# Kernel optimization log

Hardware: AMD Instinct MI355X
Metric: run time of the kernel (lower is better)

## Reference

```python
import jax, jax.numpy as jnp
import numpy as np

B, NELEC, D, NION = 2048, 32, 512, 8
NSPIN = 2
N = NELEC // NSPIN  # electrons per spin = orbital-matrix size = 16


def setup_inputs() -> dict:
    key = jax.random.key(0)
    ks = jax.random.split(key, 6)
    eq_inputs = jax.random.normal(ks[0], (B, NELEC, D), jnp.float32)
    r_ei = jax.random.normal(ks[1], (B, NELEC, NION, 3), jnp.float32)
    # learned params (stacked over the 2 spins; equal split so shapes match)
    W_lin = jax.random.normal(ks[2], (NSPIN, 2 * D, N), jnp.float32) * (0.5 / np.sqrt(D))
    b_lin = jax.random.normal(ks[3], (NSPIN, N), jnp.float32) * 0.1
    A_env = jax.random.normal(ks[4], (NSPIN, 3, 3, NION, N), jnp.float32) * 0.3
    w_ion = jax.random.normal(ks[5], (NSPIN, NION, N), jnp.float32)
    return dict(eq_inputs=eq_inputs, r_ei=r_ei, W_lin=W_lin, b_lin=b_lin,
                A_env=A_env, w_ion=w_ion)


def reference(eq_inputs, r_ei, W_lin, b_lin, A_env, w_ion):
    """Per-particle determinant antiequivariance layer.

    For each spin s and particle p, a doubly-equivariant orbital matrix
    M_p[j, k] = (y_p . W1[:,k] + y_j . W2[:,k] + b[k]) * env[j, k]
    is built (pair-concat dense split into two einsums to avoid the (B,n,n,2d)
    intermediate), with anisotropic exponential envelopes
    env[j, k] = sum_I w_ion[I,k] * exp(-||A[:,:,I,k] @ r_ei[j,I,:]||).
    Output per spin: y_p * det(M_p), stacked over spins -> (B, 2, n, d).
    """
    b, nelec, d = eq_inputs.shape
    n = nelec // NSPIN
    x = eq_inputs.reshape(b, NSPIN, n, d)            # spin_split=2 equal split
    r = r_ei.reshape(b, NSPIN, n, r_ei.shape[-2], 3)
    W1, W2 = W_lin[:, :d], W_lin[:, d:]
    # linear (doubly equivariant) part: (B, S, n_p, n_j, n_k)
    lin_p = jnp.einsum('bspf,sfk->bspk', x, W1)
    lin_j = jnp.einsum('bsjf,sfk->bsjk', x, W2) + b_lin[None, :, None, :]
    lin = lin_p[:, :, :, None, :] + lin_j[:, :, None, :, :]
    # anisotropic exponential envelopes: exp(-||A (r - R)||), combined over ions
    ar = jnp.einsum('bsjip,spqik->bsjiqk', r, A_env)        # (B,S,n,I,3,k)
    env = jnp.exp(-jnp.sqrt(jnp.sum(ar * ar, axis=-2)))     # (B,S,n,I,k)
    env = jnp.einsum('bsjik,sik->bsjk', env, w_ion)         # (B,S,n_j,n_k)
    M = lin * env[:, :, None, :, :]                         # (B,S,n_p,n_j,n_k)
    dets = jnp.linalg.det(M)                                # (B,S,n_p)
    # y_p * det(M_p), per spin (stacked over the spin axis)
    return x * dets[..., None]                              # (B,S,n,d)
```

## Files before the change

### kernel.cpp

```cpp
#include <hip/hip_runtime.h>
#include <hip/hip_bf16.h>
#include <cstdint>
#include <cstddef>

#define NSPIN 2
#define NPART 16
#define DDIM  512
#define NION  8
#define NB    4

#define RS_OFF     0
#define GRAM_OFF   1536
#define LINP_OFF   (GRAM_OFF + 1152)
#define LINJ_OFF   (LINP_OFF + 1280)
#define ENV_OFF    (LINJ_OFF + 1280)
#define DETS_OFF   (ENV_OFF + 1280)
#define LDS_FLOATS (DETS_OFF + 64)
#define LDS_BYTES  (LDS_FLOATS * 4)

#define WS_GRAM_F  16384

typedef short bf16x8 __attribute__((ext_vector_type(8)));
typedef float f32x4  __attribute__((ext_vector_type(4)));

__device__ __forceinline__ short bfc(float x) {
    unsigned u = __float_as_uint(x);
    u += 0x7FFFu + ((u >> 16) & 1u);
    return (short)(u >> 16);
}

union AFU { bf16x8 v; __hip_bfloat162 h[4]; };

__device__ __forceinline__ bf16x8 cvt8(const float4& a, const float4& b) {
    AFU u;
    u.h[0] = __float22bfloat162_rn(make_float2(a.x, a.y));
    u.h[1] = __float22bfloat162_rn(make_float2(a.z, a.w));
    u.h[2] = __float22bfloat162_rn(make_float2(b.x, b.y));
    u.h[3] = __float22bfloat162_rn(make_float2(b.z, b.w));
    return u.v;
}

#define DPPMAXU(k, ctrl) { unsigned o_ = (unsigned)__builtin_amdgcn_update_dpp(0, (int)(k), (ctrl), 0xF, 0xF, true); (k) = (k) > o_ ? (k) : o_; }

__global__ void __launch_bounds__(256)
prep_kernel(const float* __restrict__ WL, const float* __restrict__ AE,
            const float* __restrict__ WI, float* __restrict__ WSF)
{
    const int t = threadIdx.x;
    if (blockIdx.x < 16) {
        int slot = blockIdx.x * 256 + t;
        int spin = slot >> 11;
        int rem  = slot & 2047;
        int half = rem >> 10;
        int ks   = (rem >> 6) & 15;
        int lane = rem & 63;
        int cc2  = lane & 15, hh = lane >> 4;
        const float* src = WL + (size_t)spin * (2 * DDIM * NPART)
                         + ((size_t)(half * 512 + ks * 32 + hh * 8)) * NPART + cc2;
        ushort u[8];
        #pragma unroll
        for (int e = 0; e < 8; ++e) u[e] = (ushort)bfc(src[e * NPART]);
        uint4 pk;
        pk.x = (unsigned)u[0] | ((unsigned)u[1] << 16);
        pk.y = (unsigned)u[2] | ((unsigned)u[3] << 16);
        pk.z = (unsigned)u[4] | ((unsigned)u[5] << 16);
        pk.w = (unsigned)u[6] | ((unsigned)u[7] << 16);
        ((uint4*)WSF)[slot] = pk;
    } else {
        int s  = t >> 7;
        int ke = (t >> 3) & 15;
        int i  = t & 7;
        const float* Ag = AE + (size_t)s * (9 * NION * NPART);
        float a00 = Ag[((0 * 3 + 0) * NION + i) * NPART + ke];
        float a01 = Ag[((0 * 3 + 1) * NION + i) * NPART + ke];
        float a02 = Ag[((0 * 3 + 2) * NION + i) * NPART + ke];
        float a10 = Ag[((1 * 3 + 0) * NION + i) * NPART + ke];
        float a11 = Ag[((1 * 3 + 1) * NION + i) * NPART + ke];
        float a12 = Ag[((1 * 3 + 2) * NION + i) * NPART + ke];
        float a20 = Ag[((2 * 3 + 0) * NION + i) * NPART + ke];
        float a21 = Ag[((2 * 3 + 1) * NION + i) * NPART + ke];
        float a22 = Ag[((2 * 3 + 2) * NION + i) * NPART + ke];
        float* g = WSF + WS_GRAM_F + t * 8;
        g[0] = a00 * a00 + a01 * a01 + a02 * a02;
        g[1] = a10 * a10 + a11 * a11 + a12 * a12;
        g[2] = a20 * a20 + a21 * a21 + a22 * a22;
        g[3] = a00 * a10 + a01 * a11 + a02 * a12;
        g[4] = a00 * a20 + a01 * a21 + a02 * a22;
        g[5] = a10 * a20 + a11 * a21 + a12 * a22;
        g[6] = WI[(size_t)s * (NION * NPART) + i * NPART + ke];
        g[7] = 0.f;
    }
}

__global__ void __launch_bounds__(256, 4)
ppdet_kernel(const float* __restrict__ EQ, const float* __restrict__ RE,
             const float* __restrict__ WSF, const float* __restrict__ BL,
             float* __restrict__ OUT)
{
    extern __shared__ float ls[];
    const int t  = threadIdx.x;
    const int s  = blockIdx.x >> 9;
    const int b0 = (blockIdx.x & 511) * NB;

    const int l  = t & 63;
    const int w  = t >> 6;
    const int c  = l & 15;
    const int h4 = l >> 4;
    const int jr = t & 15;
    const int ke = t >> 4;

    #pragma unroll
    for (int it = 0; it < 6; ++it) {
        int idx = it * 256 + t;
        int ibuf = idx / 384, rem = idx % 384;
        int e = rem >> 4, j = rem & 15;
        ls[RS_OFF + idx] = RE[((size_t)(b0 + ibuf) * 32 + s * 16 + j) * 24 + e];
    }
    #pragma unroll
    for (int it = 0; it < 4; ++it) {
        int idx = it * 256 + t;
        int kk = idx >> 6, rem = idx & 63;
        ls[GRAM_OFF + kk * 72 + rem] = WSF[WS_GRAM_F + s * 1024 + idx];
    }

    {
        const float* xg  = EQ + ((size_t)((b0 + w) * 32 + s * 16 + c)) * DDIM + h4 * 8;
        const uint4* wb1 = (const uint4*)WSF + (size_t)s * 2048;
        const uint4* wb2 = wb1 + 1024;
        f32x4 accp = {0.f, 0.f, 0.f, 0.f}, accj = {0.f, 0.f, 0.f, 0.f};
        float4 xA[8], xB[8];
        #pragma unroll
        for (int u = 0; u < 4; ++u) {
            xA[2 * u]     = *(const float4*)(xg + u * 32);
            xA[2 * u + 1] = *(const float4*)(xg + u * 32 + 4);
        }
        #pragma unroll
        for (int kb = 0; kb < 4; ++kb) {
            float4* cur = (kb & 1) ? xB : xA;
            float4* nxt = (kb & 1) ? xA : xB;
            if (kb < 3) {
                #pragma unroll
                for (int u = 0; u < 4; ++u) {
                    nxt[2 * u]     = *(const float4*)(xg + (kb + 1) * 128 + u * 32);
                    nxt[2 * u + 1] = *(const float4*)(xg + (kb + 1) * 128 + u * 32 + 4);
                }
            }
            uint4 w1v[4], w2v[4];
            #pragma unroll
            for (int u = 0; u < 4; ++u) {
                w1v[u] = wb1[(kb * 4 + u) * 64 + l];
                w2v[u] = wb2[(kb * 4 + u) * 64 + l];
            }
            #pragma unroll
            for (int u = 0; u < 4; ++u) {
                bf16x8 af = cvt8(cur[2 * u], cur[2 * u + 1]);
                accp = __builtin_amdgcn_mfma_f32_16x16x32_bf16(af, *(bf16x8*)&w1v[u], accp, 0, 0, 0);
                accj = __builtin_amdgcn_mfma_f32_16x16x32_bf16(af, *(bf16x8*)&w2v[u], accj, 0, 0, 0);
            }
        }
        const float blv = BL[s * NPART + c];
        #pragma unroll
        for (int q = 0; q < 4; ++q) {
            ls[LINP_OFF + (w * 16 + h4 * 4 + q) * 20 + c] = accp[q];
            ls[LINJ_OFF + (w * 16 + h4 * 4 + q) * 20 + c] = accj[q] + blv;
        }
    }
    __syncthreads();

    {
        const float4* gp = (const float4*)(ls + GRAM_OFF + ke * 72);
        float ev[NB] = {0.f, 0.f, 0.f, 0.f};
        #pragma unroll
        for (int i = 0; i < 8; ++i) {
            float4 gA = gp[2 * i];
            float4 gB = gp[2 * i + 1];
            #pragma unroll
            for (int ib = 0; ib < NB; ++ib) {
                const float* rs = ls + RS_OFF + ib * 384;
                float r0 = rs[(i * 3 + 0) * 16 + jr];
                float r1 = rs[(i * 3 + 1) * 16 + jr];
                float r2 = rs[(i * 3 + 2) * 16 + jr];
                float ss = r0 * r0 * gA.x;
                ss = fmaf(r1 * r1, gA.y, ss);
                ss = fmaf(r2 * r2, gA.z, ss);
                float tcr = r0 * r1 * gA.w;
                tcr = fmaf(r0 * r2, gB.x, tcr);
                tcr = fmaf(r1 * r2, gB.y, tcr);
                ss = fmaf(2.f, tcr, ss);
                ss = fmaxf(ss, 0.f);
                ev[ib] = fmaf(gB.z, __expf(-__builtin_amdgcn_sqrtf(ss)), ev[ib]);
            }
        }
        #pragma unroll
        for (int ib = 0; ib < NB; ++ib)
            ls[ENV_OFF + (ib * 16 + jr) * 20 + ke] = ev[ib];
    }
    __syncthreads();

    const int lanebase4 = (t & 48) << 2;
    for (int ib = 0; ib < NB; ++ib) {
        float Mr[16];
        const float* lp = ls + LINP_OFF + (ib * 16 + ke) * 20;
        const float* lj = ls + LINJ_OFF + (ib * 16 + jr) * 20;
        const float* ev = ls + ENV_OFF  + (ib * 16 + jr) * 20;
        #pragma unroll
        for (int cq = 0; cq < 4; ++cq) {
            float4 a  = *(const float4*)(lp + cq * 4);
            float4 bb = *(const float4*)(lj + cq * 4);
            float4 e  = *(const float4*)(ev + cq * 4);
            Mr[cq * 4 + 0] = (a.x + bb.x) * e.x;
            Mr[cq * 4 + 1] = (a.y + bb.y) * e.y;
            Mr[cq * 4 + 2] = (a.z + bb.z) * e.z;
            Mr[cq * 4 + 3] = (a.w + bb.w) * e.w;
        }
        float detv = 1.f;
        unsigned sel = 0u;
        int inv = 0;
        bool msel = false;
        #pragma unroll
        for (int cc = 0; cc < 16; ++cc) {
            unsigned key = msel ? 0u
                : ((__float_as_uint(fabsf(Mr[cc])) & 0xFFFFFFF0u) | (unsigned)jr);
            DPPMAXU(key, 0x121); DPPMAXU(key, 0x122); DPPMAXU(key, 0x124); DPPMAXU(key, 0x128);
            const int idx = (int)(key & 15u);
            const bool ispiv = (jr == idx) && !msel;
            const int srcaddr = lanebase4 | (idx << 2);
            float Pr[16];
            #pragma unroll
            for (int k2 = cc; k2 < 16; ++k2)
                Pr[k2] = __int_as_float(__builtin_amdgcn_ds_bpermute(
                             srcaddr, __float_as_int(Mr[k2])));
            const float pv = Pr[cc];
            const float f = (msel || ispiv || pv == 0.f) ? 0.f
                          : Mr[cc] * __builtin_amdgcn_rcpf(pv);
            inv += __popc(sel >> (idx + 1));
            sel |= (1u << idx);
            msel = msel || ispiv;
            detv *= pv;
            #pragma unroll
            for (int k2 = cc + 1; k2 < 16; ++k2)
                Mr[k2] = fmaf(-f, Pr[k2], Mr[k2]);
        }
        if (inv & 1) detv = -detv;
        if (jr == 0) ls[DETS_OFF + ib * 16 + ke] = detv;
    }
    __syncthreads();

    #pragma unroll
    for (int ib = 0; ib < NB; ++ib) {
        const size_t base = ((size_t)((b0 + ib) * 32 + s * 16)) * DDIM;
        #pragma unroll
        for (int i2 = 0; i2 < 8; ++i2) {
            int f4i = i2 * 256 + t;
            float dt = ls[DETS_OFF + ib * 16 + (f4i >> 7)];
            float4 xv = ((const float4*)(EQ + base))[f4i];
            ((float4*)(OUT + base))[f4i] =
                make_float4(xv.x * dt, xv.y * dt, xv.z * dt, xv.w * dt);
        }
    }
}

extern "C" void kernel_launch(void* const* d_in, const int* in_sizes, int n_in,
                              void* d_out, int out_size, void* d_ws, size_t ws_size,
                              hipStream_t stream) {
    const float* EQ = (const float*)d_in[0];
    const float* RE = (const float*)d_in[1];
    const float* WL = (const float*)d_in[2];
    const float* BL = (const float*)d_in[3];
    const float* AE = (const float*)d_in[4];
    const float* WI = (const float*)d_in[5];
    float* OUT = (float*)d_out;
    float* WSF = (float*)d_ws;
    (void)in_sizes; (void)n_in; (void)out_size; (void)ws_size;

    prep_kernel<<<dim3(17), dim3(256), 0, stream>>>(WL, AE, WI, WSF);
    ppdet_kernel<<<dim3(1024), dim3(256), LDS_BYTES, stream>>>(EQ, RE, WSF, BL, OUT);
}
```

Measured before the change: 82.24 us.

## Make each wavefront own one batch element and drop block barriers

Restructures the kernel so that each of the four wavefronts processes its own batch element end to end, in a private LDS slice. This replaces the block-wide __syncthreads with s_waitcnt on LDS operations. r_ei rows and the Gram envelope parameters are now read directly from global memory into registers instead of being staged through LDS. The x prefetch double-buffering is removed, and output writes use nontemporal stores. The aim is to cut barrier stalls so wavefronts can progress independently, but it depends on lock-step execution within a wave for LDS visibility and loses the explicit load pipelining.

```diff
diff --git a/kernel.cpp b/kernel.cpp
--- a/kernel.cpp
+++ b/kernel.cpp
@@ -7,15 +7,9 @@
 #define NPART 16
 #define DDIM  512
 #define NION  8
-#define NB    4
-
-#define RS_OFF     0
-#define GRAM_OFF   1536
-#define LINP_OFF   (GRAM_OFF + 1152)
-#define LINJ_OFF   (LINP_OFF + 1280)
-#define ENV_OFF    (LINJ_OFF + 1280)
-#define DETS_OFF   (ENV_OFF + 1280)
-#define LDS_FLOATS (DETS_OFF + 64)
+
+#define WSLICE     976
+#define LDS_FLOATS (4 * WSLICE)
 #define LDS_BYTES  (LDS_FLOATS * 4)
 
 #define WS_GRAM_F  16384
@@ -100,60 +94,37 @@
     extern __shared__ float ls[];
     const int t  = threadIdx.x;
     const int s  = blockIdx.x >> 9;
-    const int b0 = (blockIdx.x & 511) * NB;
+    const int b0 = (blockIdx.x & 511) * 4;
 
     const int l  = t & 63;
     const int w  = t >> 6;
+    const int b  = b0 + w;
     const int c  = l & 15;
     const int h4 = l >> 4;
-    const int jr = t & 15;
-    const int ke = t >> 4;
-
-    #pragma unroll
-    for (int it = 0; it < 6; ++it) {
-        int idx = it * 256 + t;
-        int ibuf = idx / 384, rem = idx % 384;
-        int e = rem >> 4, j = rem & 15;
-        ls[RS_OFF + idx] = RE[((size_t)(b0 + ibuf) * 32 + s * 16 + j) * 24 + e];
-    }
-    #pragma unroll
-    for (int it = 0; it < 4; ++it) {
-        int idx = it * 256 + t;
-        int kk = idx >> 6, rem = idx & 63;
-        ls[GRAM_OFF + kk * 72 + rem] = WSF[WS_GRAM_F + s * 1024 + idx];
-    }
+    const int jr = l & 15;
+    const int g  = l >> 4;
+
+    float* wls = ls + w * WSLICE;
 
     {
-        const float* xg  = EQ + ((size_t)((b0 + w) * 32 + s * 16 + c)) * DDIM + h4 * 8;
+        const float* xg  = EQ + ((size_t)(b * 32 + s * 16 + c)) * DDIM + h4 * 8;
         const uint4* wb1 = (const uint4*)WSF + (size_t)s * 2048;
         const uint4* wb2 = wb1 + 1024;
         f32x4 accp = {0.f, 0.f, 0.f, 0.f}, accj = {0.f, 0.f, 0.f, 0.f};
-        float4 xA[8], xB[8];
-        #pragma unroll
-        for (int u = 0; u < 4; ++u) {
-            xA[2 * u]     = *(const float4*)(xg + u * 32);
-            xA[2 * u + 1] = *(const float4*)(xg + u * 32 + 4);
-        }
         #pragma unroll
         for (int kb = 0; kb < 4; ++kb) {
-            float4* cur = (kb & 1) ? xB : xA;
-            float4* nxt = (kb & 1) ? xA : xB;
-            if (kb < 3) {
-                #pragma unroll
-                for (int u = 0; u < 4; ++u) {
-                    nxt[2 * u]     = *(const float4*)(xg + (kb + 1) * 128 + u * 32);
-                    nxt[2 * u + 1] = *(const float4*)(xg + (kb + 1) * 128 + u * 32 + 4);
-                }
-            }
+            float4 xa[8];
             uint4 w1v[4], w2v[4];
             #pragma unroll
             for (int u = 0; u < 4; ++u) {
+                xa[2 * u]     = *(const float4*)(xg + (kb * 4 + u) * 32);
+                xa[2 * u + 1] = *(const float4*)(xg + (kb * 4 + u) * 32 + 4);
                 w1v[u] = wb1[(kb * 4 + u) * 64 + l];
                 w2v[u] = wb2[(kb * 4 + u) * 64 + l];
             }
             #pragma unroll
             for (int u = 0; u < 4; ++u) {
-                bf16x8 af = cvt8(cur[2 * u], cur[2 * u + 1]);
+                bf16x8 af = cvt8(xa[2 * u], xa[2 * u + 1]);
                 accp = __builtin_amdgcn_mfma_f32_16x16x32_bf16(af, *(bf16x8*)&w1v[u], accp, 0, 0, 0);
                 accj = __builtin_amdgcn_mfma_f32_16x16x32_bf16(af, *(bf16x8*)&w2v[u], accj, 0, 0, 0);
             }
@@ -161,25 +132,30 @@
         const float blv = BL[s * NPART + c];
         #pragma unroll
         for (int q = 0; q < 4; ++q) {
-            ls[LINP_OFF + (w * 16 + h4 * 4 + q) * 20 + c] = accp[q];
-            ls[LINJ_OFF + (w * 16 + h4 * 4 + q) * 20 + c] = accj[q] + blv;
-        }
-    }
-    __syncthreads();
+            wls[(h4 * 4 + q) * 20 + c]        = accp[q];
+            wls[320 + (h4 * 4 + q) * 20 + c]  = accj[q] + blv;
+        }
+    }
 
     {
-        const float4* gp = (const float4*)(ls + GRAM_OFF + ke * 72);
-        float ev[NB] = {0.f, 0.f, 0.f, 0.f};
-        #pragma unroll
-        for (int i = 0; i < 8; ++i) {
-            float4 gA = gp[2 * i];
-            float4 gB = gp[2 * i + 1];
-            #pragma unroll
-            for (int ib = 0; ib < NB; ++ib) {
-                const float* rs = ls + RS_OFF + ib * 384;
-                float r0 = rs[(i * 3 + 0) * 16 + jr];
-                float r1 = rs[(i * 3 + 1) * 16 + jr];
-                float r2 = rs[(i * 3 + 2) * 16 + jr];
+        float rr[24];
+        const float* rrow = RE + ((size_t)(b * 32 + s * 16 + jr)) * 24;
+        #pragma unroll
+        for (int m = 0; m < 6; ++m) {
+            float4 v = ((const float4*)rrow)[m];
+            rr[m * 4 + 0] = v.x; rr[m * 4 + 1] = v.y;
+            rr[m * 4 + 2] = v.z; rr[m * 4 + 3] = v.w;
+        }
+        #pragma unroll
+        for (int kx = 0; kx < 4; ++kx) {
+            const int ke2 = g + kx * 4;
+            const float4* gp = (const float4*)(WSF + WS_GRAM_F + s * 1024 + ke2 * 64);
+            float ev = 0.f;
+            #pragma unroll
+            for (int i = 0; i < 8; ++i) {
+                float4 gA = gp[2 * i];
+                float4 gB = gp[2 * i + 1];
+                float r0 = rr[i * 3 + 0], r1 = rr[i * 3 + 1], r2 = rr[i * 3 + 2];
                 float ss = r0 * r0 * gA.x;
                 ss = fmaf(r1 * r1, gA.y, ss);
                 ss = fmaf(r2 * r2, gA.z, ss);
@@ -188,21 +164,22 @@
                 tcr = fmaf(r1 * r2, gB.y, tcr);
                 ss = fmaf(2.f, tcr, ss);
                 ss = fmaxf(ss, 0.f);
-                ev[ib] = fmaf(gB.z, __expf(-__builtin_amdgcn_sqrtf(ss)), ev[ib]);
+                ev = fmaf(gB.z, __expf(-__builtin_amdgcn_sqrtf(ss)), ev);
             }
-        }
-        #pragma unroll
-        for (int ib = 0; ib < NB; ++ib)
-            ls[ENV_OFF + (ib * 16 + jr) * 20 + ke] = ev[ib];
-    }
-    __syncthreads();
-
-    const int lanebase4 = (t & 48) << 2;
-    for (int ib = 0; ib < NB; ++ib) {
+            wls[640 + jr * 20 + ke2] = ev;
+        }
+    }
+
+    asm volatile("s_waitcnt lgkmcnt(0)" ::: "memory");
+
+    const int lanebase4 = (l & 48) << 2;
+    #pragma unroll 1
+    for (int pp = 0; pp < 4; ++pp) {
+        const int p = pp * 4 + g;
         float Mr[16];
-        const float* lp = ls + LINP_OFF + (ib * 16 + ke) * 20;
-        const float* lj = ls + LINJ_OFF + (ib * 16 + jr) * 20;
-        const float* ev = ls + ENV_OFF  + (ib * 16 + jr) * 20;
+        const float* lp = wls + p * 20;
+        const float* lj = wls + 320 + jr * 20;
+        const float* ev = wls + 640 + jr * 20;
         #pragma unroll
         for (int cq = 0; cq < 4; ++cq) {
             float4 a  = *(const float4*)(lp + cq * 4);
@@ -242,20 +219,22 @@
                 Mr[k2] = fmaf(-f, Pr[k2], Mr[k2]);
         }
         if (inv & 1) detv = -detv;
-        if (jr == 0) ls[DETS_OFF + ib * 16 + ke] = detv;
-    }
-    __syncthreads();
-
-    #pragma unroll
-    for (int ib = 0; ib < NB; ++ib) {
-        const size_t base = ((size_t)((b0 + ib) * 32 + s * 16)) * DDIM;
-        #pragma unroll
-        for (int i2 = 0; i2 < 8; ++i2) {
-            int f4i = i2 * 256 + t;
-            float dt = ls[DETS_OFF + ib * 16 + (f4i >> 7)];
-            float4 xv = ((const float4*)(EQ + base))[f4i];
-            ((float4*)(OUT + base))[f4i] =
-                make_float4(xv.x * dt, xv.y * dt, xv.z * dt, xv.w * dt);
+        if (jr == 0) wls[960 + p] = detv;
+    }
+
+    asm volatile("s_waitcnt lgkmcnt(0)" ::: "memory");
+
+    {
+        const size_t base = ((size_t)(b * 32 + s * 16)) * DDIM;
+        const f32x4* src4 = (const f32x4*)(EQ + base);
+        f32x4* dst4 = (f32x4*)(OUT + base);
+        #pragma unroll
+        for (int i2 = 0; i2 < 32; ++i2) {
+            int f4i = i2 * 64 + l;
+            float dt = wls[960 + (f4i >> 7)];
+            f32x4 xv = src4[f4i];
+            f32x4 o = xv * dt;
+            __builtin_nontemporal_store(o, dst4 + f4i);
         }
     }
 }
```

Result: no change. 83.53 us (+1.6%).
